# Performance work log

Hardware: AMD Instinct MI355X
Metric: run time of the kernel (lower is better)

The kernel has to match this reference:

```python
import jax, jax.numpy as jnp
import numpy as np

B, C, H, W = 2, 64, 64, 64
DH = C // 2  # 32, projected channel dim

def setup_inputs() -> dict:
    key = jax.random.key(0)
    ks = jax.random.split(key, 9)
    x = jax.random.normal(ks[0], (B, C, H, W), dtype=jnp.float32)
    # 1x1 conv weights stored as [out_ch, in_ch] (kernel dims squeezed)
    w1 = jax.random.normal(ks[1], (DH, C), dtype=jnp.float32) * 0.05
    b1 = jax.random.normal(ks[2], (DH,), dtype=jnp.float32) * 0.05
    w2 = jax.random.normal(ks[3], (DH, C), dtype=jnp.float32) * 0.05
    b2 = jax.random.normal(ks[4], (DH,), dtype=jnp.float32) * 0.05
    w3 = jax.random.normal(ks[5], (DH, C), dtype=jnp.float32) * 0.05
    b3 = jax.random.normal(ks[6], (DH,), dtype=jnp.float32) * 0.05
    w4 = jax.random.normal(ks[7], (C, DH), dtype=jnp.float32) * 0.05
    b4 = jax.random.normal(ks[8], (C,), dtype=jnp.float32) * 0.05
    return {"x": x, "w1": w1, "b1": b1, "w2": w2, "b2": b2,
            "w3": w3, "b3": b3, "w4": w4, "b4": b4}

def _proj(x, w, b):
    # 1x1 conv then permute(0,2,3,1) then flatten(B,H,W) -> [N, DH]
    y = jnp.einsum('bchw,oc->bhwo', x, w) + b
    return y.reshape(-1, w.shape[0])

def reference(x, w1, b1, w2, b2, w3, b3, w4, b4):
    b_, c_, h_, w_ = x.shape
    q = _proj(x, w1, b1)   # [N, DH]
    k = _proj(x, w2, b2)   # [N, DH]
    v = _proj(x, w3, b3)   # [N, DH]
    att = q @ k.T                       # [N, N]
    att = jax.nn.softmax(att, axis=0)   # softmax over dim 0 (rows, per column)
    o = att @ v                         # [N, DH]
    o = o.reshape(b_, h_, w_, c_ // 2)
    # conv4 (1x1) on [B, DH, H, W] then residual
    y = jnp.einsum('bhwc,oc->bohw', o, w4) + b4[None, :, None, None]
    return y + x
```

## Files before the change

kernel.cpp:

```cpp
#include <hip/hip_runtime.h>
#include <hip/hip_bf16.h>

#define N_TOK   8192
#define DH      32
#define CCH     64
#define HWSZ    4096
#define LOG2E   1.4426950408889634f
#define NCH_Z   32
#define NCH_O   32
#define ITILE   64

typedef __attribute__((ext_vector_type(8))) short  bf16x8;
typedef __attribute__((ext_vector_type(4))) short  bf16x4;
typedef __attribute__((ext_vector_type(4))) float  f32x4;

static __device__ __forceinline__ short f2bf(float f) {
    __hip_bfloat16 h = __float2bfloat16(f);
    return __builtin_bit_cast(short, h);
}
static __device__ __forceinline__ float bf2f(short s) {
    unsigned u = ((unsigned)(unsigned short)s) << 16;
    return __builtin_bit_cast(float, u);
}

static __device__ __forceinline__ bf16x8 load_frag8(const __hip_bfloat16* __restrict__ base,
                                                    int row0, int l) {
    const __hip_bfloat16* p = base + (size_t)(row0 + (l & 15)) * DH + ((l >> 4) << 3);
    return *reinterpret_cast<const bf16x8*>(p);
}

__global__ __launch_bounds__(256) void k_qkv(
        const float* __restrict__ x,
        const float* __restrict__ w1, const float* __restrict__ b1,
        const float* __restrict__ w2, const float* __restrict__ b2,
        const float* __restrict__ w3, const float* __restrict__ b3,
        __hip_bfloat16* __restrict__ Qb, __hip_bfloat16* __restrict__ Kb,
        __hip_bfloat16* __restrict__ VTb) {
    __shared__ float4 w1s[16][32];
    __shared__ float4 w2s[16][32];
    __shared__ float4 w3s[16][32];
    __shared__ short  vt[32][8];
    int t = threadIdx.x;
    for (int i = t; i < 512; i += 256) {
        int cg = i >> 5, d = i & 31;
        w1s[cg][d] = *reinterpret_cast<const float4*>(w1 + d * CCH + cg * 4);
        w2s[cg][d] = *reinterpret_cast<const float4*>(w2 + d * CCH + cg * 4);
        w3s[cg][d] = *reinterpret_cast<const float4*>(w3 + d * CCH + cg * 4);
    }
    __syncthreads();
    int d = t & 31, nr = t >> 5;
    int n0 = blockIdx.x * 8;
    int n = n0 + nr;
    int b = n >> 12, hw = n & 4095;
    const float* xp = x + (size_t)b * (CCH * HWSZ) + hw;
    float aq = b1[d], ak = b2[d], av = b3[d];
    #pragma unroll
    for (int cg = 0; cg < 16; ++cg) {
        float x0 = xp[(cg * 4 + 0) * HWSZ];
        float x1 = xp[(cg * 4 + 1) * HWSZ];
        float x2 = xp[(cg * 4 + 2) * HWSZ];
        float x3 = xp[(cg * 4 + 3) * HWSZ];
        float4 a = w1s[cg][d];
        aq = fmaf(a.x, x0, aq); aq = fmaf(a.y, x1, aq);
        aq = fmaf(a.z, x2, aq); aq = fmaf(a.w, x3, aq);
        float4 bb = w2s[cg][d];
        ak = fmaf(bb.x, x0, ak); ak = fmaf(bb.y, x1, ak);
        ak = fmaf(bb.z, x2, ak); ak = fmaf(bb.w, x3, ak);
        float4 cc = w3s[cg][d];
        av = fmaf(cc.x, x0, av); av = fmaf(cc.y, x1, av);
        av = fmaf(cc.z, x2, av); av = fmaf(cc.w, x3, av);
    }
    Qb[(size_t)n * DH + d] = __float2bfloat16(aq * LOG2E);
    Kb[(size_t)n * DH + d] = __float2bfloat16(ak);
    vt[d][nr] = f2bf(av);
    __syncthreads();
    if (t < 32) {
        bf16x8 row = *reinterpret_cast<const bf16x8*>(&vt[t][0]);
        *reinterpret_cast<bf16x8*>(VTb + (size_t)t * N_TOK + n0) = row;
    }
}

__global__ __launch_bounds__(256) void k_zpart(
        const __hip_bfloat16* __restrict__ Qb, const __hip_bfloat16* __restrict__ Kb,
        float* __restrict__ Zpart) {
    int l  = threadIdx.x & 63;
    int gw = blockIdx.x * 4 + (threadIdx.x >> 6);
    int jt = gw >> 5;
    int ic = gw & 31;
    int j0 = jt * 64;
    const int ilen = N_TOK / NCH_Z;
    int i0 = ic * ilen;
    bf16x8 ka[4];
    #pragma unroll
    for (int f = 0; f < 4; ++f) ka[f] = load_frag8(Kb, j0 + f * 16, l);
    float zac[16];
    #pragma unroll
    for (int t = 0; t < 16; ++t) zac[t] = 0.f;
    const f32x4 z4 = {0.f, 0.f, 0.f, 0.f};
    #pragma unroll 2
    for (int i = i0; i < i0 + ilen; i += 16) {
        bf16x8 qf = load_frag8(Qb, i, l);
        #pragma unroll
        for (int f = 0; f < 4; ++f) {
            f32x4 s = __builtin_amdgcn_mfma_f32_16x16x32_bf16(ka[f], qf, z4, 0, 0, 0);
            #pragma unroll
            for (int r = 0; r < 4; ++r)
                zac[f * 4 + r] += __builtin_amdgcn_exp2f(s[r]);
        }
    }
    #pragma unroll
    for (int t = 0; t < 16; ++t) {
        float z = zac[t];
        z += __shfl_xor(z, 1); z += __shfl_xor(z, 2);
        z += __shfl_xor(z, 4); z += __shfl_xor(z, 8);
        zac[t] = z;
    }
    if ((l & 15) == 0) {
        int jr = (l >> 4) * 4;
        #pragma unroll
        for (int f = 0; f < 4; ++f)
            #pragma unroll
            for (int r = 0; r < 4; ++r)
                Zpart[(size_t)ic * N_TOK + j0 + f * 16 + jr + r] = zac[f * 4 + r];
    }
}

__global__ __launch_bounds__(256) void k_attn(
        const __hip_bfloat16* __restrict__ Qb, const __hip_bfloat16* __restrict__ Kb,
        const __hip_bfloat16* __restrict__ VTb, const float* __restrict__ Zpart,
        __hip_bfloat16* __restrict__ oTp) {
    __shared__ float rzs[256];
    int t = threadIdx.x;
    int jc  = blockIdx.x & 31;
    int itg = blockIdx.x >> 5;
    const int jlen = N_TOK / NCH_O;
    int j0c = jc * jlen;
    {
        float z = 0.f;
        #pragma unroll 8
        for (int c = 0; c < NCH_Z; ++c) z += Zpart[(size_t)c * N_TOK + j0c + t];
        rzs[t] = __builtin_amdgcn_rcpf(z);
    }
    __syncthreads();
    int l = t & 63;
    int it = itg * 4 + (t >> 6);
    int i0 = it * ITILE;
    bf16x8 qb[4];
    #pragma unroll
    for (int f = 0; f < 4; ++f) qb[f] = load_frag8(Qb, i0 + f * 16, l);
    f32x4 acc0[4], acc1[4];
    #pragma unroll
    for (int f = 0; f < 4; ++f) { acc0[f] = {0.f,0.f,0.f,0.f}; acc1[f] = {0.f,0.f,0.f,0.f}; }
    const f32x4 z4 = {0.f, 0.f, 0.f, 0.f};
    int lo16 = l & 15, hi4 = (l >> 4) << 2;
    const __hip_bfloat16* v0p = VTb + (size_t)lo16 * N_TOK;
    const __hip_bfloat16* v1p = VTb + (size_t)(lo16 + 16) * N_TOK;
    #pragma unroll 2
    for (int jl = 0; jl < jlen; jl += 16) {
        int j = j0c + jl;
        f32x4 rz = *reinterpret_cast<const f32x4*>(&rzs[jl + hi4]);
        bf16x8 kaf = load_frag8(Kb, j, l);
        bf16x4 va0 = *reinterpret_cast<const bf16x4*>(v0p + j + hi4);
        bf16x4 va1 = *reinterpret_cast<const bf16x4*>(v1p + j + hi4);
        #pragma unroll
        for (int f = 0; f < 4; ++f) {
            f32x4 s = __builtin_amdgcn_mfma_f32_16x16x32_bf16(kaf, qb[f], z4, 0, 0, 0);
            bf16x4 e;
            #pragma unroll
            for (int r = 0; r < 4; ++r)
                e[r] = f2bf(__builtin_amdgcn_exp2f(s[r]) * rz[r]);
            acc0[f] = __builtin_amdgcn_mfma_f32_16x16x16bf16_1k(va0, e, acc0[f], 0, 0, 0);
            acc1[f] = __builtin_amdgcn_mfma_f32_16x16x16bf16_1k(va1, e, acc1[f], 0, 0, 0);
        }
    }
    int icol = i0 + lo16;
    #pragma unroll
    for (int f = 0; f < 4; ++f) {
        #pragma unroll
        for (int r = 0; r < 4; ++r) {
            oTp[(size_t)(jc * DH + hi4 + r)      * N_TOK + icol + f * 16] =
                __float2bfloat16(acc0[f][r]);
            oTp[(size_t)(jc * DH + 16 + hi4 + r) * N_TOK + icol + f * 16] =
                __float2bfloat16(acc1[f][r]);
        }
    }
}

__global__ __launch_bounds__(256) void k_fin(
        const __hip_bfloat16* __restrict__ oTp, const float* __restrict__ w4,
        const float* __restrict__ b4, const float* __restrict__ x,
        float* __restrict__ y) {
    __shared__ float w4s[64][32];
    __shared__ float tile[32][36];
    int t = threadIdx.x;
    {
        const float4* w4v = reinterpret_cast<const float4*>(w4);
        float4* dst = reinterpret_cast<float4*>(&w4s[0][0]);
        dst[t * 2]     = w4v[t * 2];
        dst[t * 2 + 1] = w4v[t * 2 + 1];
    }
    int n0 = blockIdx.x * 32;
    int d = t >> 3, seg = t & 7;
    float s[4];
    #pragma unroll
    for (int k = 0; k < 4; ++k) s[k] = 0.f;
    #pragma unroll 4
    for (int c = 0; c < NCH_O; ++c) {
        bf16x4 v = *reinterpret_cast<const bf16x4*>(
            oTp + ((size_t)c * DH + d) * N_TOK + n0 + seg * 4);
        #pragma unroll
        for (int k = 0; k < 4; ++k) s[k] += bf2f(v[k]);
    }
    #pragma unroll
    for (int k = 0; k < 4; ++k) tile[d][seg * 4 + k] = s[k];
    __syncthreads();
    int n_l = t & 31, cg = t >> 5;
    int n = n0 + n_l, b = n >> 12, hw = n & 4095;
    #pragma unroll
    for (int ci = 0; ci < 8; ++ci) {
        int c = cg * 8 + ci;
        float acc = b4[c];
        #pragma unroll
        for (int dd = 0; dd < 32; ++dd)
            acc = fmaf(w4s[c][dd], tile[dd][n_l], acc);
        int idx = b * (CCH * HWSZ) + c * HWSZ + hw;
        y[idx] = acc + x[idx];
    }
}

extern "C" void kernel_launch(void* const* d_in, const int* in_sizes, int n_in,
                              void* d_out, int out_size, void* d_ws, size_t ws_size,
                              hipStream_t stream) {
    const float* x  = (const float*)d_in[0];
    const float* w1 = (const float*)d_in[1];
    const float* b1 = (const float*)d_in[2];
    const float* w2 = (const float*)d_in[3];
    const float* b2 = (const float*)d_in[4];
    const float* w3 = (const float*)d_in[5];
    const float* b3 = (const float*)d_in[6];
    const float* w4 = (const float*)d_in[7];
    const float* b4 = (const float*)d_in[8];
    float* y = (float*)d_out;

    char* ws = (char*)d_ws;
    const size_t KB = 1024;
    __hip_bfloat16* Qb  = (__hip_bfloat16*)(ws);
    __hip_bfloat16* Kb  = (__hip_bfloat16*)(ws + 512 * KB);
    __hip_bfloat16* VTb = (__hip_bfloat16*)(ws + 1024 * KB);
    float*          Zp  = (float*)(ws + 1536 * KB);
    __hip_bfloat16* oTp = (__hip_bfloat16*)(ws + 2560 * KB);

    hipLaunchKernelGGL(k_qkv,   dim3(N_TOK / 8), dim3(256), 0, stream,
                       x, w1, b1, w2, b2, w3, b3, Qb, Kb, VTb);
    hipLaunchKernelGGL(k_zpart, dim3(1024), dim3(256), 0, stream, Qb, Kb, Zp);
    hipLaunchKernelGGL(k_attn,  dim3(1024), dim3(256), 0, stream,
                       Qb, Kb, VTb, Zp, oTp);
    hipLaunchKernelGGL(k_fin,   dim3(N_TOK / 32), dim3(256), 0, stream,
                       oTp, w4, b4, x, y);
}
```

Measured before the change: 67.42 us.

## Fuse four kernels into one cooperative persistent kernel with grid syncs

Replaces the four separate launches (QKV projection, softmax denominator partials, attention, output projection) with a single cooperative kernel of 512 persistent blocks. The blocks loop over each phase's work and separate phases with grid.sync(). The aim is to remove per-launch overhead and inter-kernel gaps. The cost is grid-wide barrier latency and fewer resident blocks (512 instead of 1024) for the heavier phases. If the cooperative launch fails, it falls back to the original four-kernel path.

```diff
diff --git a/kernel.cpp b/kernel.cpp
--- a/kernel.cpp
+++ b/kernel.cpp
@@ -1,5 +1,8 @@
 #include <hip/hip_runtime.h>
+#include <hip/hip_cooperative_groups.h>
 #include <hip/hip_bf16.h>
+
+namespace cg = cooperative_groups;
 
 #define N_TOK   8192
 #define DH      32
@@ -9,6 +12,7 @@
 #define NCH_Z   32
 #define NCH_O   32
 #define ITILE   64
+#define GRID_CP 512
 
 typedef __attribute__((ext_vector_type(8))) short  bf16x8;
 typedef __attribute__((ext_vector_type(4))) short  bf16x4;
@@ -27,6 +31,218 @@
                                                     int row0, int l) {
     const __hip_bfloat16* p = base + (size_t)(row0 + (l & 15)) * DH + ((l >> 4) << 3);
     return *reinterpret_cast<const bf16x8*>(p);
+}
+
+__global__ __launch_bounds__(256, 2) void k_fused(
+        const float* __restrict__ x,
+        const float* __restrict__ w1, const float* __restrict__ b1,
+        const float* __restrict__ w2, const float* __restrict__ b2,
+        const float* __restrict__ w3, const float* __restrict__ b3,
+        const float* __restrict__ w4, const float* __restrict__ b4,
+        __hip_bfloat16* __restrict__ Qb, __hip_bfloat16* __restrict__ Kb,
+        __hip_bfloat16* __restrict__ VTb, float* __restrict__ Zp,
+        __hip_bfloat16* __restrict__ oTp, float* __restrict__ y) {
+    __shared__ __align__(16) char smem[25088];
+    cg::grid_group grid = cg::this_grid();
+    const int t   = threadIdx.x;
+    const int blk = blockIdx.x;
+    const int ng  = gridDim.x;
+
+    {
+        float4 (*w1s)[32] = (float4(*)[32])(smem);
+        float4 (*w2s)[32] = (float4(*)[32])(smem + 8192);
+        float4 (*w3s)[32] = (float4(*)[32])(smem + 16384);
+        short  (*vt)[8]   = (short (*)[8])(smem + 24576);
+        for (int i = t; i < 512; i += 256) {
+            int cg_ = i >> 5, d = i & 31;
+            w1s[cg_][d] = *reinterpret_cast<const float4*>(w1 + d * CCH + cg_ * 4);
+            w2s[cg_][d] = *reinterpret_cast<const float4*>(w2 + d * CCH + cg_ * 4);
+            w3s[cg_][d] = *reinterpret_cast<const float4*>(w3 + d * CCH + cg_ * 4);
+        }
+        __syncthreads();
+        int d = t & 31, nr = t >> 5;
+        for (int u = blk; u < N_TOK / 8; u += ng) {
+            int n0 = u * 8;
+            int n = n0 + nr;
+            int b = n >> 12, hw = n & 4095;
+            const float* xp = x + (size_t)b * (CCH * HWSZ) + hw;
+            float aq = b1[d], ak = b2[d], av = b3[d];
+            #pragma unroll
+            for (int cg_ = 0; cg_ < 16; ++cg_) {
+                float x0 = xp[(cg_ * 4 + 0) * HWSZ];
+                float x1 = xp[(cg_ * 4 + 1) * HWSZ];
+                float x2 = xp[(cg_ * 4 + 2) * HWSZ];
+                float x3 = xp[(cg_ * 4 + 3) * HWSZ];
+                float4 a = w1s[cg_][d];
+                aq = fmaf(a.x, x0, aq); aq = fmaf(a.y, x1, aq);
+                aq = fmaf(a.z, x2, aq); aq = fmaf(a.w, x3, aq);
+                float4 bb = w2s[cg_][d];
+                ak = fmaf(bb.x, x0, ak); ak = fmaf(bb.y, x1, ak);
+                ak = fmaf(bb.z, x2, ak); ak = fmaf(bb.w, x3, ak);
+                float4 cc = w3s[cg_][d];
+                av = fmaf(cc.x, x0, av); av = fmaf(cc.y, x1, av);
+                av = fmaf(cc.z, x2, av); av = fmaf(cc.w, x3, av);
+            }
+            Qb[(size_t)n * DH + d] = __float2bfloat16(aq * LOG2E);
+            Kb[(size_t)n * DH + d] = __float2bfloat16(ak);
+            vt[d][nr] = f2bf(av);
+            __syncthreads();
+            if (t < 32) {
+                bf16x8 row = *reinterpret_cast<const bf16x8*>(&vt[t][0]);
+                *reinterpret_cast<bf16x8*>(VTb + (size_t)t * N_TOK + n0) = row;
+            }
+            __syncthreads();
+        }
+    }
+    grid.sync();
+
+    {
+        int l = t & 63, w = t >> 6;
+        const int ilen = N_TOK / NCH_Z;
+        const f32x4 z4 = {0.f, 0.f, 0.f, 0.f};
+        for (int u = blk * 4 + w; u < 128 * NCH_Z; u += ng * 4) {
+            int jt = u >> 5;
+            int ic = u & 31;
+            int j0 = jt * 64;
+            int i0 = ic * ilen;
+            bf16x8 ka[4];
+            #pragma unroll
+            for (int f = 0; f < 4; ++f) ka[f] = load_frag8(Kb, j0 + f * 16, l);
+            float zac[16];
+            #pragma unroll
+            for (int k = 0; k < 16; ++k) zac[k] = 0.f;
+            #pragma unroll 2
+            for (int i = i0; i < i0 + ilen; i += 16) {
+                bf16x8 qf = load_frag8(Qb, i, l);
+                #pragma unroll
+                for (int f = 0; f < 4; ++f) {
+                    f32x4 s = __builtin_amdgcn_mfma_f32_16x16x32_bf16(ka[f], qf, z4, 0, 0, 0);
+                    #pragma unroll
+                    for (int r = 0; r < 4; ++r)
+                        zac[f * 4 + r] += __builtin_amdgcn_exp2f(s[r]);
+                }
+            }
+            #pragma unroll
+            for (int k = 0; k < 16; ++k) {
+                float z = zac[k];
+                z += __shfl_xor(z, 1); z += __shfl_xor(z, 2);
+                z += __shfl_xor(z, 4); z += __shfl_xor(z, 8);
+                zac[k] = z;
+            }
+            if ((l & 15) == 0) {
+                int jr = (l >> 4) * 4;
+                #pragma unroll
+                for (int f = 0; f < 4; ++f)
+                    #pragma unroll
+                    for (int r = 0; r < 4; ++r)
+                        Zp[(size_t)ic * N_TOK + j0 + f * 16 + jr + r] = zac[f * 4 + r];
+            }
+        }
+    }
+    grid.sync();
+
+    {
+        float* rzs = (float*)smem;
+        const int jlen = N_TOK / NCH_O;
+        const f32x4 z4 = {0.f, 0.f, 0.f, 0.f};
+        int l = t & 63;
+        int lo16 = l & 15, hi4 = (l >> 4) << 2;
+        const __hip_bfloat16* v0p = VTb + (size_t)lo16 * N_TOK;
+        const __hip_bfloat16* v1p = VTb + (size_t)(lo16 + 16) * N_TOK;
+        for (int u = blk; u < 1024; u += ng) {
+            int jc  = u & 31;
+            int itg = u >> 5;
+            int j0c = jc * jlen;
+            {
+                float z = 0.f;
+                #pragma unroll 8
+                for (int c = 0; c < NCH_Z; ++c) z += Zp[(size_t)c * N_TOK + j0c + t];
+                rzs[t] = __builtin_amdgcn_rcpf(z);
+            }
+            __syncthreads();
+            int it = itg * 4 + (t >> 6);
+            int i0 = it * ITILE;
+            bf16x8 qb[4];
+            #pragma unroll
+            for (int f = 0; f < 4; ++f) qb[f] = load_frag8(Qb, i0 + f * 16, l);
+            f32x4 acc0[4], acc1[4];
+            #pragma unroll
+            for (int f = 0; f < 4; ++f) { acc0[f] = {0.f,0.f,0.f,0.f}; acc1[f] = {0.f,0.f,0.f,0.f}; }
+            #pragma unroll 2
+            for (int jl = 0; jl < jlen; jl += 16) {
+                int j = j0c + jl;
+                f32x4 rz = *reinterpret_cast<const f32x4*>(&rzs[jl + hi4]);
+                bf16x8 kaf = load_frag8(Kb, j, l);
+                bf16x4 va0 = *reinterpret_cast<const bf16x4*>(v0p + j + hi4);
+                bf16x4 va1 = *reinterpret_cast<const bf16x4*>(v1p + j + hi4);
+                #pragma unroll
+                for (int f = 0; f < 4; ++f) {
+                    f32x4 s = __builtin_amdgcn_mfma_f32_16x16x32_bf16(kaf, qb[f], z4, 0, 0, 0);
+                    bf16x4 e;
+                    #pragma unroll
+                    for (int r = 0; r < 4; ++r)
+                        e[r] = f2bf(__builtin_amdgcn_exp2f(s[r]) * rz[r]);
+                    acc0[f] = __builtin_amdgcn_mfma_f32_16x16x16bf16_1k(va0, e, acc0[f], 0, 0, 0);
+                    acc1[f] = __builtin_amdgcn_mfma_f32_16x16x16bf16_1k(va1, e, acc1[f], 0, 0, 0);
+                }
+            }
+            int icol = i0 + lo16;
+            #pragma unroll
+            for (int f = 0; f < 4; ++f) {
+                #pragma unroll
+                for (int r = 0; r < 4; ++r) {
+                    oTp[(size_t)(jc * DH + hi4 + r)      * N_TOK + icol + f * 16] =
+                        __float2bfloat16(acc0[f][r]);
+                    oTp[(size_t)(jc * DH + 16 + hi4 + r) * N_TOK + icol + f * 16] =
+                        __float2bfloat16(acc1[f][r]);
+                }
+            }
+            __syncthreads();
+        }
+    }
+    grid.sync();
+
+    {
+        float (*w4s)[32]  = (float(*)[32])(smem);
+        float (*tile)[36] = (float(*)[36])(smem + 8192);
+        {
+            const float4* w4v = reinterpret_cast<const float4*>(w4);
+            float4* dst = reinterpret_cast<float4*>(&w4s[0][0]);
+            dst[t * 2]     = w4v[t * 2];
+            dst[t * 2 + 1] = w4v[t * 2 + 1];
+        }
+        __syncthreads();
+        for (int u = blk; u < 256; u += ng) {
+            int n0 = u * 32;
+            int d = t >> 3, seg = t & 7;
+            float s[4];
+            #pragma unroll
+            for (int k = 0; k < 4; ++k) s[k] = 0.f;
+            #pragma unroll 4
+            for (int c = 0; c < NCH_O; ++c) {
+                bf16x4 v = *reinterpret_cast<const bf16x4*>(
+                    oTp + ((size_t)c * DH + d) * N_TOK + n0 + seg * 4);
+                #pragma unroll
+                for (int k = 0; k < 4; ++k) s[k] += bf2f(v[k]);
+            }
+            #pragma unroll
+            for (int k = 0; k < 4; ++k) tile[d][seg * 4 + k] = s[k];
+            __syncthreads();
+            int n_l = t & 31, cgr = t >> 5;
+            int n = n0 + n_l, b = n >> 12, hw = n & 4095;
+            #pragma unroll
+            for (int ci = 0; ci < 8; ++ci) {
+                int c = cgr * 8 + ci;
+                float acc = b4[c];
+                #pragma unroll
+                for (int dd = 0; dd < 32; ++dd)
+                    acc = fmaf(w4s[c][dd], tile[dd][n_l], acc);
+                int idx = b * (CCH * HWSZ) + c * HWSZ + hw;
+                y[idx] = acc + x[idx];
+            }
+            __syncthreads();
+        }
+    }
 }
 
 __global__ __launch_bounds__(256) void k_qkv(
@@ -42,10 +258,10 @@
     __shared__ short  vt[32][8];
     int t = threadIdx.x;
     for (int i = t; i < 512; i += 256) {
-        int cg = i >> 5, d = i & 31;
-        w1s[cg][d] = *reinterpret_cast<const float4*>(w1 + d * CCH + cg * 4);
-        w2s[cg][d] = *reinterpret_cast<const float4*>(w2 + d * CCH + cg * 4);
-        w3s[cg][d] = *reinterpret_cast<const float4*>(w3 + d * CCH + cg * 4);
+        int cg_ = i >> 5, d = i & 31;
+        w1s[cg_][d] = *reinterpret_cast<const float4*>(w1 + d * CCH + cg_ * 4);
+        w2s[cg_][d] = *reinterpret_cast<const float4*>(w2 + d * CCH + cg_ * 4);
+        w3s[cg_][d] = *reinterpret_cast<const float4*>(w3 + d * CCH + cg_ * 4);
     }
     __syncthreads();
     int d = t & 31, nr = t >> 5;
@@ -55,18 +271,18 @@
     const float* xp = x + (size_t)b * (CCH * HWSZ) + hw;
     float aq = b1[d], ak = b2[d], av = b3[d];
     #pragma unroll
-    for (int cg = 0; cg < 16; ++cg) {
-        float x0 = xp[(cg * 4 + 0) * HWSZ];
-        float x1 = xp[(cg * 4 + 1) * HWSZ];
-        float x2 = xp[(cg * 4 + 2) * HWSZ];
-        float x3 = xp[(cg * 4 + 3) * HWSZ];
-        float4 a = w1s[cg][d];
+    for (int cg_ = 0; cg_ < 16; ++cg_) {
+        float x0 = xp[(cg_ * 4 + 0) * HWSZ];
+        float x1 = xp[(cg_ * 4 + 1) * HWSZ];
+        float x2 = xp[(cg_ * 4 + 2) * HWSZ];
+        float x3 = xp[(cg_ * 4 + 3) * HWSZ];
+        float4 a = w1s[cg_][d];
         aq = fmaf(a.x, x0, aq); aq = fmaf(a.y, x1, aq);
         aq = fmaf(a.z, x2, aq); aq = fmaf(a.w, x3, aq);
-        float4 bb = w2s[cg][d];
+        float4 bb = w2s[cg_][d];
         ak = fmaf(bb.x, x0, ak); ak = fmaf(bb.y, x1, ak);
         ak = fmaf(bb.z, x2, ak); ak = fmaf(bb.w, x3, ak);
-        float4 cc = w3s[cg][d];
+        float4 cc = w3s[cg_][d];
         av = fmaf(cc.x, x0, av); av = fmaf(cc.y, x1, av);
         av = fmaf(cc.z, x2, av); av = fmaf(cc.w, x3, av);
     }
@@ -95,7 +311,7 @@
     for (int f = 0; f < 4; ++f) ka[f] = load_frag8(Kb, j0 + f * 16, l);
     float zac[16];
     #pragma unroll
-    for (int t = 0; t < 16; ++t) zac[t] = 0.f;
+    for (int k = 0; k < 16; ++k) zac[k] = 0.f;
     const f32x4 z4 = {0.f, 0.f, 0.f, 0.f};
     #pragma unroll 2
     for (int i = i0; i < i0 + ilen; i += 16) {
@@ -109,11 +325,11 @@
         }
     }
     #pragma unroll
-    for (int t = 0; t < 16; ++t) {
-        float z = zac[t];
+    for (int k = 0; k < 16; ++k) {
+        float z = zac[k];
         z += __shfl_xor(z, 1); z += __shfl_xor(z, 2);
         z += __shfl_xor(z, 4); z += __shfl_xor(z, 8);
-        zac[t] = z;
+        zac[k] = z;
     }
     if ((l & 15) == 0) {
         int jr = (l >> 4) * 4;
@@ -214,11 +430,11 @@
     #pragma unroll
     for (int k = 0; k < 4; ++k) tile[d][seg * 4 + k] = s[k];
     __syncthreads();
-    int n_l = t & 31, cg = t >> 5;
+    int n_l = t & 31, cgr = t >> 5;
     int n = n0 + n_l, b = n >> 12, hw = n & 4095;
     #pragma unroll
     for (int ci = 0; ci < 8; ++ci) {
-        int c = cg * 8 + ci;
+        int c = cgr * 8 + ci;
         float acc = b4[c];
         #pragma unroll
         for (int dd = 0; dd < 32; ++dd)
@@ -250,11 +466,20 @@
     float*          Zp  = (float*)(ws + 1536 * KB);
     __hip_bfloat16* oTp = (__hip_bfloat16*)(ws + 2560 * KB);
 
-    hipLaunchKernelGGL(k_qkv,   dim3(N_TOK / 8), dim3(256), 0, stream,
-                       x, w1, b1, w2, b2, w3, b3, Qb, Kb, VTb);
-    hipLaunchKernelGGL(k_zpart, dim3(1024), dim3(256), 0, stream, Qb, Kb, Zp);
-    hipLaunchKernelGGL(k_attn,  dim3(1024), dim3(256), 0, stream,
-                       Qb, Kb, VTb, Zp, oTp);
-    hipLaunchKernelGGL(k_fin,   dim3(N_TOK / 32), dim3(256), 0, stream,
-                       oTp, w4, b4, x, y);
-}
+    void* args[] = { (void*)&x, (void*)&w1, (void*)&b1, (void*)&w2, (void*)&b2,
+                     (void*)&w3, (void*)&b3, (void*)&w4, (void*)&b4,
+                     (void*)&Qb, (void*)&Kb, (void*)&VTb, (void*)&Zp,
+                     (void*)&oTp, (void*)&y };
+    hipError_t err = hipLaunchCooperativeKernel((const void*)k_fused,
+                                                dim3(GRID_CP), dim3(256),
+                                                args, 0, stream);
+    if (err != hipSuccess) {
+        hipLaunchKernelGGL(k_qkv,   dim3(N_TOK / 8), dim3(256), 0, stream,
+                           x, w1, b1, w2, b2, w3, b3, Qb, Kb, VTb);
+        hipLaunchKernelGGL(k_zpart, dim3(1024), dim3(256), 0, stream, Qb, Kb, Zp);
+        hipLaunchKernelGGL(k_attn,  dim3(1024), dim3(256), 0, stream,
+                           Qb, Kb, VTb, Zp, oTp);
+        hipLaunchKernelGGL(k_fin,   dim3(N_TOK / 32), dim3(256), 0, stream,
+                           oTp, w4, b4, x, y);
+    }
+}
```

Result: slower. 245.6 us (+264.3%).

## Retile Z and attention kernels into 16 chunks with 1024-thread blocks

Applied to the files above, without the earlier changes.

The column-sum and attention kernels are regridded. Each now uses 256 blocks of 16 waves over 16 chunks of 512 tokens, and each wave owns a 32-column or 32-row tile instead of 64. This halves the number of partial Z sums and partial outputs that k_attn and k_fin must reduce, which cuts partial-buffer traffic. In exchange, each wave reuses its K/Q fragments over fewer MFMAs, and the bigger blocks may change occupancy and latency hiding.

```diff
diff --git a/kernel.cpp b/kernel.cpp
--- a/kernel.cpp
+++ b/kernel.cpp
@@ -6,9 +6,8 @@
 #define CCH     64
 #define HWSZ    4096
 #define LOG2E   1.4426950408889634f
-#define NCH_Z   32
-#define NCH_O   32
-#define ITILE   64
+#define NCH     16
+#define CLEN    512
 
 typedef __attribute__((ext_vector_type(8))) short  bf16x8;
 typedef __attribute__((ext_vector_type(4))) short  bf16x4;
@@ -80,109 +79,101 @@
     }
 }
 
-__global__ __launch_bounds__(256) void k_zpart(
+__global__ __launch_bounds__(1024) void k_z(
         const __hip_bfloat16* __restrict__ Qb, const __hip_bfloat16* __restrict__ Kb,
-        float* __restrict__ Zpart) {
-    int l  = threadIdx.x & 63;
-    int gw = blockIdx.x * 4 + (threadIdx.x >> 6);
-    int jt = gw >> 5;
-    int ic = gw & 31;
-    int j0 = jt * 64;
-    const int ilen = N_TOK / NCH_Z;
-    int i0 = ic * ilen;
-    bf16x8 ka[4];
-    #pragma unroll
-    for (int f = 0; f < 4; ++f) ka[f] = load_frag8(Kb, j0 + f * 16, l);
-    float zac[16];
-    #pragma unroll
-    for (int t = 0; t < 16; ++t) zac[t] = 0.f;
+        float* __restrict__ Zp) {
+    int t = threadIdx.x;
+    int l = t & 63, w = t >> 6;
+    int ic = blockIdx.x >> 4;
+    int jg = blockIdx.x & 15;
+    int j0 = jg * CLEN + w * 32;
+    int i0 = ic * CLEN;
+    bf16x8 ka0 = load_frag8(Kb, j0, l);
+    bf16x8 ka1 = load_frag8(Kb, j0 + 16, l);
+    float zac[8];
+    #pragma unroll
+    for (int k = 0; k < 8; ++k) zac[k] = 0.f;
     const f32x4 z4 = {0.f, 0.f, 0.f, 0.f};
     #pragma unroll 2
-    for (int i = i0; i < i0 + ilen; i += 16) {
+    for (int i = i0; i < i0 + CLEN; i += 16) {
         bf16x8 qf = load_frag8(Qb, i, l);
-        #pragma unroll
-        for (int f = 0; f < 4; ++f) {
-            f32x4 s = __builtin_amdgcn_mfma_f32_16x16x32_bf16(ka[f], qf, z4, 0, 0, 0);
-            #pragma unroll
-            for (int r = 0; r < 4; ++r)
-                zac[f * 4 + r] += __builtin_amdgcn_exp2f(s[r]);
+        f32x4 s0 = __builtin_amdgcn_mfma_f32_16x16x32_bf16(ka0, qf, z4, 0, 0, 0);
+        f32x4 s1 = __builtin_amdgcn_mfma_f32_16x16x32_bf16(ka1, qf, z4, 0, 0, 0);
+        #pragma unroll
+        for (int r = 0; r < 4; ++r) {
+            zac[r]     += __builtin_amdgcn_exp2f(s0[r]);
+            zac[4 + r] += __builtin_amdgcn_exp2f(s1[r]);
         }
     }
     #pragma unroll
-    for (int t = 0; t < 16; ++t) {
-        float z = zac[t];
+    for (int k = 0; k < 8; ++k) {
+        float z = zac[k];
         z += __shfl_xor(z, 1); z += __shfl_xor(z, 2);
         z += __shfl_xor(z, 4); z += __shfl_xor(z, 8);
-        zac[t] = z;
+        zac[k] = z;
     }
     if ((l & 15) == 0) {
         int jr = (l >> 4) * 4;
         #pragma unroll
-        for (int f = 0; f < 4; ++f)
-            #pragma unroll
-            for (int r = 0; r < 4; ++r)
-                Zpart[(size_t)ic * N_TOK + j0 + f * 16 + jr + r] = zac[f * 4 + r];
-    }
-}
-
-__global__ __launch_bounds__(256) void k_attn(
+        for (int r = 0; r < 4; ++r) {
+            Zp[(size_t)ic * N_TOK + j0 + jr + r]      = zac[r];
+            Zp[(size_t)ic * N_TOK + j0 + 16 + jr + r] = zac[4 + r];
+        }
+    }
+}
+
+__global__ __launch_bounds__(1024) void k_af(
         const __hip_bfloat16* __restrict__ Qb, const __hip_bfloat16* __restrict__ Kb,
-        const __hip_bfloat16* __restrict__ VTb, const float* __restrict__ Zpart,
+        const __hip_bfloat16* __restrict__ VTb, const float* __restrict__ Zp,
         __hip_bfloat16* __restrict__ oTp) {
-    __shared__ float rzs[256];
-    int t = threadIdx.x;
-    int jc  = blockIdx.x & 31;
-    int itg = blockIdx.x >> 5;
-    const int jlen = N_TOK / NCH_O;
-    int j0c = jc * jlen;
-    {
+    __shared__ float rzs[CLEN];
+    int t = threadIdx.x;
+    int l = t & 63, w = t >> 6;
+    int rg = blockIdx.x >> 4;
+    int jc = blockIdx.x & 15;
+    int j0c = jc * CLEN;
+    if (t < CLEN) {
         float z = 0.f;
-        #pragma unroll 8
-        for (int c = 0; c < NCH_Z; ++c) z += Zpart[(size_t)c * N_TOK + j0c + t];
+        #pragma unroll
+        for (int c = 0; c < NCH; ++c) z += Zp[(size_t)c * N_TOK + j0c + t];
         rzs[t] = __builtin_amdgcn_rcpf(z);
     }
     __syncthreads();
-    int l = t & 63;
-    int it = itg * 4 + (t >> 6);
-    int i0 = it * ITILE;
-    bf16x8 qb[4];
-    #pragma unroll
-    for (int f = 0; f < 4; ++f) qb[f] = load_frag8(Qb, i0 + f * 16, l);
-    f32x4 acc0[4], acc1[4];
-    #pragma unroll
-    for (int f = 0; f < 4; ++f) { acc0[f] = {0.f,0.f,0.f,0.f}; acc1[f] = {0.f,0.f,0.f,0.f}; }
+    int i0 = rg * CLEN + w * 32;
+    bf16x8 qb0 = load_frag8(Qb, i0, l);
+    bf16x8 qb1 = load_frag8(Qb, i0 + 16, l);
+    f32x4 a00 = {0.f,0.f,0.f,0.f}, a01 = a00, a10 = a00, a11 = a00;
     const f32x4 z4 = {0.f, 0.f, 0.f, 0.f};
     int lo16 = l & 15, hi4 = (l >> 4) << 2;
     const __hip_bfloat16* v0p = VTb + (size_t)lo16 * N_TOK;
     const __hip_bfloat16* v1p = VTb + (size_t)(lo16 + 16) * N_TOK;
     #pragma unroll 2
-    for (int jl = 0; jl < jlen; jl += 16) {
+    for (int jl = 0; jl < CLEN; jl += 16) {
         int j = j0c + jl;
         f32x4 rz = *reinterpret_cast<const f32x4*>(&rzs[jl + hi4]);
         bf16x8 kaf = load_frag8(Kb, j, l);
         bf16x4 va0 = *reinterpret_cast<const bf16x4*>(v0p + j + hi4);
         bf16x4 va1 = *reinterpret_cast<const bf16x4*>(v1p + j + hi4);
-        #pragma unroll
-        for (int f = 0; f < 4; ++f) {
-            f32x4 s = __builtin_amdgcn_mfma_f32_16x16x32_bf16(kaf, qb[f], z4, 0, 0, 0);
-            bf16x4 e;
-            #pragma unroll
-            for (int r = 0; r < 4; ++r)
-                e[r] = f2bf(__builtin_amdgcn_exp2f(s[r]) * rz[r]);
-            acc0[f] = __builtin_amdgcn_mfma_f32_16x16x16bf16_1k(va0, e, acc0[f], 0, 0, 0);
-            acc1[f] = __builtin_amdgcn_mfma_f32_16x16x16bf16_1k(va1, e, acc1[f], 0, 0, 0);
+        f32x4 s0 = __builtin_amdgcn_mfma_f32_16x16x32_bf16(kaf, qb0, z4, 0, 0, 0);
+        f32x4 s1 = __builtin_amdgcn_mfma_f32_16x16x32_bf16(kaf, qb1, z4, 0, 0, 0);
+        bf16x4 e0, e1;
+        #pragma unroll
+        for (int r = 0; r < 4; ++r) {
+            e0[r] = f2bf(__builtin_amdgcn_exp2f(s0[r]) * rz[r]);
+            e1[r] = f2bf(__builtin_amdgcn_exp2f(s1[r]) * rz[r]);
         }
+        a00 = __builtin_amdgcn_mfma_f32_16x16x16bf16_1k(va0, e0, a00, 0, 0, 0);
+        a01 = __builtin_amdgcn_mfma_f32_16x16x16bf16_1k(va1, e0, a01, 0, 0, 0);
+        a10 = __builtin_amdgcn_mfma_f32_16x16x16bf16_1k(va0, e1, a10, 0, 0, 0);
+        a11 = __builtin_amdgcn_mfma_f32_16x16x16bf16_1k(va1, e1, a11, 0, 0, 0);
     }
     int icol = i0 + lo16;
     #pragma unroll
-    for (int f = 0; f < 4; ++f) {
-        #pragma unroll
-        for (int r = 0; r < 4; ++r) {
-            oTp[(size_t)(jc * DH + hi4 + r)      * N_TOK + icol + f * 16] =
-                __float2bfloat16(acc0[f][r]);
-            oTp[(size_t)(jc * DH + 16 + hi4 + r) * N_TOK + icol + f * 16] =
-                __float2bfloat16(acc1[f][r]);
-        }
+    for (int r = 0; r < 4; ++r) {
+        oTp[(size_t)(jc * DH + hi4 + r)      * N_TOK + icol]      = __float2bfloat16(a00[r]);
+        oTp[(size_t)(jc * DH + 16 + hi4 + r) * N_TOK + icol]      = __float2bfloat16(a01[r]);
+        oTp[(size_t)(jc * DH + hi4 + r)      * N_TOK + icol + 16] = __float2bfloat16(a10[r]);
+        oTp[(size_t)(jc * DH + 16 + hi4 + r) * N_TOK + icol + 16] = __float2bfloat16(a11[r]);
     }
 }
 
@@ -205,7 +196,7 @@
     #pragma unroll
     for (int k = 0; k < 4; ++k) s[k] = 0.f;
     #pragma unroll 4
-    for (int c = 0; c < NCH_O; ++c) {
+    for (int c = 0; c < NCH; ++c) {
         bf16x4 v = *reinterpret_cast<const bf16x4*>(
             oTp + ((size_t)c * DH + d) * N_TOK + n0 + seg * 4);
         #pragma unroll
@@ -214,11 +205,11 @@
     #pragma unroll
     for (int k = 0; k < 4; ++k) tile[d][seg * 4 + k] = s[k];
     __syncthreads();
-    int n_l = t & 31, cg = t >> 5;
+    int n_l = t & 31, cgr = t >> 5;
     int n = n0 + n_l, b = n >> 12, hw = n & 4095;
     #pragma unroll
     for (int ci = 0; ci < 8; ++ci) {
-        int c = cg * 8 + ci;
+        int c = cgr * 8 + ci;
         float acc = b4[c];
         #pragma unroll
         for (int dd = 0; dd < 32; ++dd)
@@ -248,13 +239,13 @@
     __hip_bfloat16* Kb  = (__hip_bfloat16*)(ws + 512 * KB);
     __hip_bfloat16* VTb = (__hip_bfloat16*)(ws + 1024 * KB);
     float*          Zp  = (float*)(ws + 1536 * KB);
-    __hip_bfloat16* oTp = (__hip_bfloat16*)(ws + 2560 * KB);
-
-    hipLaunchKernelGGL(k_qkv,   dim3(N_TOK / 8), dim3(256), 0, stream,
+    __hip_bfloat16* oTp = (__hip_bfloat16*)(ws + 2048 * KB);
+
+    hipLaunchKernelGGL(k_qkv, dim3(N_TOK / 8), dim3(256), 0, stream,
                        x, w1, b1, w2, b2, w3, b3, Qb, Kb, VTb);
-    hipLaunchKernelGGL(k_zpart, dim3(1024), dim3(256), 0, stream, Qb, Kb, Zp);
-    hipLaunchKernelGGL(k_attn,  dim3(1024), dim3(256), 0, stream,
+    hipLaunchKernelGGL(k_z,   dim3(256), dim3(1024), 0, stream, Qb, Kb, Zp);
+    hipLaunchKernelGGL(k_af,  dim3(256), dim3(1024), 0, stream,
                        Qb, Kb, VTb, Zp, oTp);
-    hipLaunchKernelGGL(k_fin,   dim3(N_TOK / 32), dim3(256), 0, stream,
+    hipLaunchKernelGGL(k_fin, dim3(N_TOK / 32), dim3(256), 0, stream,
                        oTp, w4, b4, x, y);
 }
```

Result: slower. 80.75 us (+19.8%).
